# Optimization experiments

Measured on AMD Instinct MI355X. Metric: run time of the kernel, lower is better.

Reference implementation:

```python
import jax, jax.numpy as jnp
import numpy as np
import math

SQRT5 = math.sqrt(5.0)


def setup_inputs() -> dict:
    key = jax.random.key(0)
    k1, k2, k3, k4 = jax.random.split(key, 4)
    N1, N2, D = 8192, 8192, 64
    X1 = jax.random.normal(k1, (N1, D), dtype=jnp.float32)
    X2 = jax.random.normal(k2, (N2, D), dtype=jnp.float32)
    # positive scaling / lengthscale, kept away from 0 for numerical sanity
    c = jax.random.uniform(k3, (1,), dtype=jnp.float32) + 0.5
    l = jax.random.uniform(k4, (D,), dtype=jnp.float32) + 0.5
    return {"X1": X1, "X2": X2, "c": c, "l": l}


def _matern52(X1, X2, c, l):
    X1_l = X1 / l  # [N1, D]
    X2_l = X2 / l  # [N2, D]
    # pairwise Euclidean distance via the expansion ||a-b||^2 = ||a||^2 + ||b||^2 - 2 a.b
    # (avoids materializing the [N1, N2, D] broadcasted difference tensor)
    sq1 = jnp.sum(X1_l * X1_l, axis=-1)  # [N1]
    sq2 = jnp.sum(X2_l * X2_l, axis=-1)  # [N2]
    cross = jnp.einsum("nd,md->nm", X1_l, X2_l)  # [N1, N2]
    d2 = jnp.maximum(sq1[:, None] + sq2[None, :] - 2.0 * cross, 0.0)
    r = jnp.sqrt(d2)  # [N1, N2]
    c2 = jnp.squeeze(c * c)
    return c2 * (1.0 + SQRT5 * r + (5.0 / 3.0) * (r * r)) * jnp.exp(-SQRT5 * r)


def reference(X1, X2, c, l):
    return _matern52(X1, X2, c, l)
```

## Files before the change

### kernel.cpp

```cpp
#include <hip/hip_runtime.h>
#include <math.h>

#define N_DIM 64
#define TILE  128

typedef unsigned short ushort_t;
typedef unsigned int   uint_t;
typedef _Float16 f16x8 __attribute__((ext_vector_type(8)));
typedef _Float16 f16x4 __attribute__((ext_vector_type(4)));
typedef float    f32x4 __attribute__((ext_vector_type(4)));

__device__ __forceinline__ int swz16(int row, int kc) {
    return (row << 7) + ((kc ^ (row & 7)) << 4);
}

typedef __attribute__((address_space(1))) const void gas_void;
typedef __attribute__((address_space(3))) void       las_void;
__device__ __forceinline__ void gload16(const void* g, void* l) {
    __builtin_amdgcn_global_load_lds((gas_void*)g, (las_void*)l, 16, 0, 0);
}

__global__ __launch_bounds__(256)
void matern52_prep_kernel(const float* __restrict__ X,
                          const float* __restrict__ l,
                          unsigned char* __restrict__ dst,
                          float* __restrict__ sq, int N)
{
    const int t   = threadIdx.x;
    const int kq  = t & 15;
    const int row = blockIdx.x * 16 + (t >> 4);

    float4 lv = *reinterpret_cast<const float4*>(&l[kq * 4]);
    float4 x  = *reinterpret_cast<const float4*>(&X[(size_t)row * N_DIM + kq * 4]);
    const float a0 = x.x / lv.x, a1 = x.y / lv.y, a2 = x.z / lv.z, a3 = x.w / lv.w;

    float s = a0 * a0;
    s = fmaf(a1, a1, s); s = fmaf(a2, a2, s); s = fmaf(a3, a3, s);
    s += __shfl_xor(s, 1);
    s += __shfl_xor(s, 2);
    s += __shfl_xor(s, 4);
    s += __shfl_xor(s, 8);
    if (kq == 0) sq[row] = s;

    f16x4 h = { (_Float16)a0, (_Float16)a1, (_Float16)a2, (_Float16)a3 };
    const int off = (row << 7) + ((((kq >> 1) ^ (row & 7))) << 4) + ((kq & 1) << 3);
    *reinterpret_cast<f16x4*>(dst + off) = h;
}

__global__ __launch_bounds__(256, 4)
void matern52_main_kernel(const unsigned char* __restrict__ A16,
                          const unsigned char* __restrict__ B16,
                          const float* __restrict__ sq1,
                          const float* __restrict__ sq2,
                          const float* __restrict__ cc,
                          float* __restrict__ out,
                          int N1, int N2)
{
    __shared__ __align__(16) unsigned char lds[2 * TILE * N_DIM * 2];

    const int t  = threadIdx.x;
    const int bi = blockIdx.y, bj = blockIdx.x;

    unsigned char* ldsA = lds;
    unsigned char* ldsB = lds + TILE * N_DIM * 2;

    {
        const unsigned char* srcA = A16 + (size_t)bi * (TILE * N_DIM * 2);
        const unsigned char* srcB = B16 + (size_t)bj * (TILE * N_DIM * 2);
        const int wbase = (t >> 6) << 10;
        const int gb    = t * 16;
        #pragma unroll
        for (int i = 0; i < 4; ++i) {
            gload16(srcA + i * 4096 + gb, ldsA + i * 4096 + wbase);
            gload16(srcB + i * 4096 + gb, ldsB + i * 4096 + wbase);
        }
    }
    __syncthreads();

    const int wid  = t >> 6;
    const int lane = t & 63;
    const int wtr  = wid >> 1;
    const int wtc  = wid & 1;
    const int fr   = lane & 15;
    const int kg   = lane >> 4;

    f32x4 acc[4][4] = {};

    #pragma unroll
    for (int kk = 0; kk < 2; ++kk) {
        f16x8 af[4], bg[4];
        #pragma unroll
        for (int m = 0; m < 4; ++m)
            af[m] = *reinterpret_cast<const f16x8*>(
                ldsA + swz16(wtr * 64 + m * 16 + fr, kk * 4 + kg));
        #pragma unroll
        for (int n = 0; n < 4; ++n)
            bg[n] = *reinterpret_cast<const f16x8*>(
                ldsB + swz16(wtc * 64 + n * 16 + fr, kk * 4 + kg));
        #pragma unroll
        for (int m = 0; m < 4; ++m)
            #pragma unroll
            for (int n = 0; n < 4; ++n)
                acc[m][n] = __builtin_amdgcn_mfma_f32_16x16x32_f16(
                    bg[n], af[m], acc[m][n], 0, 0, 0);
    }

    const float c0 = cc[0];
    const float SQ5    = 2.23606797749979f;
    const float FIVE3  = 1.66666666666667f;
    const float NK     = -3.22617785847899f;
    const float l2c2   = 2.885390081777927f * __logf(c0);

    const float* sqA = sq1 + bi * TILE;
    const float* sqB = sq2 + bj * TILE + wtc * 64;

    #pragma unroll
    for (int m = 0; m < 4; ++m) {
        const int row_l = wtr * 64 + m * 16 + fr;
        const float sa = sqA[row_l];
        float* rowp = out + ((size_t)(bi * TILE) + row_l) * (size_t)N2
                          + (size_t)(bj * TILE) + wtc * 64;
        #pragma unroll
        for (int n = 0; n < 4; ++n) {
            const int cb = n * 16 + kg * 4;
            f32x4 sb4 = *reinterpret_cast<const f32x4*>(sqB + cb);
            f32x4 v = acc[m][n];
            f32x4 res;
            #pragma unroll
            for (int q = 0; q < 4; ++q) {
                float d2 = fmaxf(fmaf(-2.0f, v[q], sa + sb4[q]), 0.0f);
                float r  = __builtin_amdgcn_sqrtf(d2);
                float e  = __builtin_amdgcn_exp2f(fmaf(NK, r, l2c2));
                res[q] = fmaf(FIVE3, d2, fmaf(SQ5, r, 1.0f)) * e;
            }
            *reinterpret_cast<f32x4*>(rowp + cb) = res;
        }
    }
}

__device__ __forceinline__ ushort_t f2bf(float f) {
    uint_t u = __float_as_uint(f);
    u += 0x7FFFu + ((u >> 16) & 1u);
    return (ushort_t)(u >> 16);
}
__device__ __forceinline__ float bf2f(ushort_t h) {
    return __uint_as_float(((uint_t)h) << 16);
}
typedef short s16x8 __attribute__((ext_vector_type(8)));

__global__ __launch_bounds__(512, 4)
void matern52_fallback_kernel(const float* __restrict__ X1,
                              const float* __restrict__ X2,
                              const float* __restrict__ cc,
                              const float* __restrict__ l,
                              float* __restrict__ out,
                              int N1, int N2)
{
    __shared__ ushort_t Ah[TILE * N_DIM], Al[TILE * N_DIM];
    __shared__ ushort_t Bh[TILE * N_DIM], Bl[TILE * N_DIM];
    __shared__ float sqA[TILE], sqB[TILE];

    const int t  = threadIdx.x;
    const int bi = blockIdx.y, bj = blockIdx.x;
    const int kq   = t & 15;
    const int rsub = t >> 4;

    float4 lv = *reinterpret_cast<const float4*>(&l[kq * 4]);
    const float rlx = 1.f / lv.x, rly = 1.f / lv.y, rlz = 1.f / lv.z, rlw = 1.f / lv.w;
    const float* x1b = X1 + (size_t)(bi * TILE) * N_DIM;
    const float* x2b = X2 + (size_t)(bj * TILE) * N_DIM;

    #define STAGE(Xb, Th, Tl, SQ)                                              \
    {                                                                          \
        _Pragma("unroll")                                                      \
        for (int c = 0; c < 4; ++c) {                                          \
            const int row = c * 32 + rsub;                                     \
            float4 x = *reinterpret_cast<const float4*>(&(Xb)[row * N_DIM + kq * 4]); \
            float a0 = x.x * rlx, a1 = x.y * rly, a2 = x.z * rlz, a3 = x.w * rlw; \
            ushort_t h0 = f2bf(a0), h1 = f2bf(a1), h2 = f2bf(a2), h3 = f2bf(a3); \
            ushort_t e0 = f2bf(a0 - bf2f(h0)), e1 = f2bf(a1 - bf2f(h1));       \
            ushort_t e2 = f2bf(a2 - bf2f(h2)), e3 = f2bf(a3 - bf2f(h3));       \
            const int off = (row << 7) + (((kq >> 1) << 4) ^ ((row & 7) << 4)) + ((kq & 1) << 3); \
            uint2 hv, lvv;                                                     \
            hv.x  = (uint_t)h0 | ((uint_t)h1 << 16);                           \
            hv.y  = (uint_t)h2 | ((uint_t)h3 << 16);                           \
            lvv.x = (uint_t)e0 | ((uint_t)e1 << 16);                           \
            lvv.y = (uint_t)e2 | ((uint_t)e3 << 16);                           \
            *reinterpret_cast<uint2*>((char*)(Th) + off) = hv;                 \
            *reinterpret_cast<uint2*>((char*)(Tl) + off) = lvv;                \
            float s = a0 * a0;                                                 \
            s = fmaf(a1, a1, s); s = fmaf(a2, a2, s); s = fmaf(a3, a3, s);     \
            s += __shfl_xor(s, 1);                                             \
            s += __shfl_xor(s, 2);                                             \
            s += __shfl_xor(s, 4);                                             \
            s += __shfl_xor(s, 8);                                             \
            if (kq == 0) (SQ)[row] = s;                                        \
        }                                                                      \
    }
    STAGE(x1b, Ah, Al, sqA)
    STAGE(x2b, Bh, Bl, sqB)
    #undef STAGE
    __syncthreads();

    const int wid  = t >> 6;
    const int lane = t & 63;
    const int wtr = wid >> 1, wtc = wid & 1;
    const int fr  = lane & 15, kg = lane >> 4;

    f32x4 acc[2][4] = {};
    #pragma unroll
    for (int pass = 0; pass < 3; ++pass) {
        const ushort_t* TA = (pass == 2) ? Al : Ah;
        const ushort_t* TB = (pass == 1) ? Bl : Bh;
        #pragma unroll
        for (int kk = 0; kk < 2; ++kk) {
            s16x8 af[2], bg[4];
            #pragma unroll
            for (int m = 0; m < 2; ++m)
                af[m] = *reinterpret_cast<const s16x8*>(
                    (const char*)TA + swz16(wtr * 32 + m * 16 + fr, kk * 4 + kg));
            #pragma unroll
            for (int n = 0; n < 4; ++n)
                bg[n] = *reinterpret_cast<const s16x8*>(
                    (const char*)TB + swz16(wtc * 64 + n * 16 + fr, kk * 4 + kg));
            #pragma unroll
            for (int m = 0; m < 2; ++m)
                #pragma unroll
                for (int n = 0; n < 4; ++n)
                    acc[m][n] = __builtin_amdgcn_mfma_f32_16x16x32_bf16(
                        bg[n], af[m], acc[m][n], 0, 0, 0);
        }
    }

    const float c0 = cc[0];
    const float SQ5   = 2.23606797749979f;
    const float FIVE3 = 1.66666666666667f;
    const float lnc2  = 2.0f * __logf(c0);

    #pragma unroll
    for (int m = 0; m < 2; ++m) {
        const int row_l = wtr * 32 + m * 16 + fr;
        const float sa = sqA[row_l];
        float* rowp = out + ((size_t)(bi * TILE) + row_l) * (size_t)N2
                          + (size_t)(bj * TILE) + wtc * 64;
        #pragma unroll
        for (int n = 0; n < 4; ++n) {
            const int cb = n * 16 + kg * 4;
            f32x4 sb4 = *reinterpret_cast<const f32x4*>(&sqB[wtc * 64 + cb]);
            f32x4 v = acc[m][n];
            f32x4 res;
            #pragma unroll
            for (int q = 0; q < 4; ++q) {
                float d2 = fmaxf(fmaf(-2.0f, v[q], sa + sb4[q]), 0.0f);
                float r  = sqrtf(d2);
                float e  = __expf(fmaf(-SQ5, r, lnc2));
                res[q] = fmaf(FIVE3, d2, fmaf(SQ5, r, 1.0f)) * e;
            }
            *reinterpret_cast<f32x4*>(rowp + cb) = res;
        }
    }
}

extern "C" void kernel_launch(void* const* d_in, const int* in_sizes, int n_in,
                              void* d_out, int out_size, void* d_ws, size_t ws_size,
                              hipStream_t stream) {
    const float* X1 = (const float*)d_in[0];
    const float* X2 = (const float*)d_in[1];
    const float* c  = (const float*)d_in[2];
    const float* l  = (const float*)d_in[3];
    float* out = (float*)d_out;

    const int N1 = in_sizes[0] / N_DIM;
    const int N2 = in_sizes[1] / N_DIM;

    const size_t aBytes = (size_t)N1 * 128;
    const size_t bBytes = (size_t)N2 * 128;
    const size_t needWs = aBytes + bBytes + (size_t)(N1 + N2) * sizeof(float);

    dim3 grid(N2 / TILE, N1 / TILE);

    if (ws_size >= needWs) {
        unsigned char* A16 = (unsigned char*)d_ws;
        unsigned char* B16 = A16 + aBytes;
        float* sq1 = (float*)(B16 + bBytes);
        float* sq2 = sq1 + N1;

        matern52_prep_kernel<<<dim3(N1 / 16), 256, 0, stream>>>(X1, l, A16, sq1, N1);
        matern52_prep_kernel<<<dim3(N2 / 16), 256, 0, stream>>>(X2, l, B16, sq2, N2);
        matern52_main_kernel<<<grid, 256, 0, stream>>>(A16, B16, sq1, sq2, c, out, N1, N2);
    } else {
        matern52_fallback_kernel<<<grid, 512, 0, stream>>>(X1, X2, c, l, out, N1, N2);
    }
}
```

Baseline: 58.13 us.

## Read f16 operands directly from global memory and use nontemporal output stores

The main kernel no longer stages A/B tiles into LDS through global_load_lds with a swizzled layout and a barrier. Each lane now loads its MFMA fragments straight from global memory, which relies on L1/L2 caching of the small f16 operand arrays. The prep kernel writes a plain row-major layout to match. Output stores become nontemporal to avoid polluting cache with the 256MB result. The trade-off is redundant global/L2 traffic for operand fragments, since each tile is read by several waves, in exchange for dropping the LDS staging and the sync.

```diff
diff --git a/kernel.cpp b/kernel.cpp
--- a/kernel.cpp
+++ b/kernel.cpp
@@ -9,16 +9,6 @@
 typedef _Float16 f16x8 __attribute__((ext_vector_type(8)));
 typedef _Float16 f16x4 __attribute__((ext_vector_type(4)));
 typedef float    f32x4 __attribute__((ext_vector_type(4)));
-
-__device__ __forceinline__ int swz16(int row, int kc) {
-    return (row << 7) + ((kc ^ (row & 7)) << 4);
-}
-
-typedef __attribute__((address_space(1))) const void gas_void;
-typedef __attribute__((address_space(3))) void       las_void;
-__device__ __forceinline__ void gload16(const void* g, void* l) {
-    __builtin_amdgcn_global_load_lds((gas_void*)g, (las_void*)l, 16, 0, 0);
-}
 
 __global__ __launch_bounds__(256)
 void matern52_prep_kernel(const float* __restrict__ X,
@@ -43,8 +33,7 @@
     if (kq == 0) sq[row] = s;
 
     f16x4 h = { (_Float16)a0, (_Float16)a1, (_Float16)a2, (_Float16)a3 };
-    const int off = (row << 7) + ((((kq >> 1) ^ (row & 7))) << 4) + ((kq & 1) << 3);
-    *reinterpret_cast<f16x4*>(dst + off) = h;
+    *reinterpret_cast<f16x4*>(dst + (size_t)row * 128 + kq * 8) = h;
 }
 
 __global__ __launch_bounds__(256, 4)
@@ -56,27 +45,8 @@
                           float* __restrict__ out,
                           int N1, int N2)
 {
-    __shared__ __align__(16) unsigned char lds[2 * TILE * N_DIM * 2];
-
-    const int t  = threadIdx.x;
-    const int bi = blockIdx.y, bj = blockIdx.x;
-
-    unsigned char* ldsA = lds;
-    unsigned char* ldsB = lds + TILE * N_DIM * 2;
-
-    {
-        const unsigned char* srcA = A16 + (size_t)bi * (TILE * N_DIM * 2);
-        const unsigned char* srcB = B16 + (size_t)bj * (TILE * N_DIM * 2);
-        const int wbase = (t >> 6) << 10;
-        const int gb    = t * 16;
-        #pragma unroll
-        for (int i = 0; i < 4; ++i) {
-            gload16(srcA + i * 4096 + gb, ldsA + i * 4096 + wbase);
-            gload16(srcB + i * 4096 + gb, ldsB + i * 4096 + wbase);
-        }
-    }
-    __syncthreads();
-
+    const int t    = threadIdx.x;
+    const int bi   = blockIdx.y, bj = blockIdx.x;
     const int wid  = t >> 6;
     const int lane = t & 63;
     const int wtr  = wid >> 1;
@@ -84,6 +54,11 @@
     const int fr   = lane & 15;
     const int kg   = lane >> 4;
 
+    const unsigned char* pa =
+        A16 + (size_t)bi * (TILE * 128) + ((wtr * 64 + fr) << 7) + (kg << 4);
+    const unsigned char* pb =
+        B16 + (size_t)bj * (TILE * 128) + ((wtc * 64 + fr) << 7) + (kg << 4);
+
     f32x4 acc[4][4] = {};
 
     #pragma unroll
@@ -91,12 +66,10 @@
         f16x8 af[4], bg[4];
         #pragma unroll
         for (int m = 0; m < 4; ++m)
-            af[m] = *reinterpret_cast<const f16x8*>(
-                ldsA + swz16(wtr * 64 + m * 16 + fr, kk * 4 + kg));
+            af[m] = *reinterpret_cast<const f16x8*>(pa + m * 2048 + kk * 64);
         #pragma unroll
         for (int n = 0; n < 4; ++n)
-            bg[n] = *reinterpret_cast<const f16x8*>(
-                ldsB + swz16(wtc * 64 + n * 16 + fr, kk * 4 + kg));
+            bg[n] = *reinterpret_cast<const f16x8*>(pb + n * 2048 + kk * 64);
         #pragma unroll
         for (int m = 0; m < 4; ++m)
             #pragma unroll
@@ -106,10 +79,10 @@
     }
 
     const float c0 = cc[0];
-    const float SQ5    = 2.23606797749979f;
-    const float FIVE3  = 1.66666666666667f;
-    const float NK     = -3.22617785847899f;
-    const float l2c2   = 2.885390081777927f * __logf(c0);
+    const float SQ5   = 2.23606797749979f;
+    const float FIVE3 = 1.66666666666667f;
+    const float NK    = -3.22617785847899f;
+    const float l2c2  = 2.885390081777927f * __logf(c0);
 
     const float* sqA = sq1 + bi * TILE;
     const float* sqB = sq2 + bj * TILE + wtc * 64;
@@ -133,7 +106,7 @@
                 float e  = __builtin_amdgcn_exp2f(fmaf(NK, r, l2c2));
                 res[q] = fmaf(FIVE3, d2, fmaf(SQ5, r, 1.0f)) * e;
             }
-            *reinterpret_cast<f32x4*>(rowp + cb) = res;
+            __builtin_nontemporal_store(res, reinterpret_cast<f32x4*>(rowp + cb));
         }
     }
 }
@@ -147,6 +120,10 @@
     return __uint_as_float(((uint_t)h) << 16);
 }
 typedef short s16x8 __attribute__((ext_vector_type(8)));
+
+__device__ __forceinline__ int swz16(int row, int kc) {
+    return (row << 7) + ((kc ^ (row & 7)) << 4);
+}
 
 __global__ __launch_bounds__(512, 4)
 void matern52_fallback_kernel(const float* __restrict__ X1,
```

Result: slower. 91.62 us (+57.6%).

## Make main kernel persistent over four B tiles with double-buffered LDS prefetch

Applied to the files above, without the earlier changes.

Each 512-thread block now loads a 256-row A tile once and loops over four consecutive 128-column B tiles. Two B buffers let the next-next tile's global_load_lds overlap the epilogue of the current tile. This amortizes the A load and the launch/prologue cost across more output and hides B load latency behind the exp/sqrt epilogue and stores. In exchange the block uses 64 KB of LDS, which lowers occupancy, and there are fewer blocks (512 for the test shape). It also adds a shape guard that falls back to the old path for unsupported sizes.

```diff
diff --git a/kernel.cpp b/kernel.cpp
--- a/kernel.cpp
+++ b/kernel.cpp
@@ -3,6 +3,9 @@
 
 #define N_DIM 64
 #define TILE  128
+#define BM    256
+#define BN    128
+#define NTJ   4
 
 typedef unsigned short ushort_t;
 typedef unsigned int   uint_t;
@@ -47,32 +50,38 @@
     *reinterpret_cast<f16x4*>(dst + off) = h;
 }
 
-__global__ __launch_bounds__(256, 4)
+__global__ __launch_bounds__(512, 4)
 void matern52_main_kernel(const unsigned char* __restrict__ A16,
                           const unsigned char* __restrict__ B16,
                           const float* __restrict__ sq1,
                           const float* __restrict__ sq2,
                           const float* __restrict__ cc,
                           float* __restrict__ out,
-                          int N1, int N2)
+                          int N1, int N2, int njg)
 {
-    __shared__ __align__(16) unsigned char lds[2 * TILE * N_DIM * 2];
-
-    const int t  = threadIdx.x;
-    const int bi = blockIdx.y, bj = blockIdx.x;
-
+    __shared__ __align__(16) unsigned char lds[65536];
     unsigned char* ldsA = lds;
-    unsigned char* ldsB = lds + TILE * N_DIM * 2;
+
+    const int t    = threadIdx.x;
+    const int bi   = blockIdx.x / njg;
+    const int bjg  = blockIdx.x % njg;
+    const int bj0  = bjg * NTJ;
+
+    const int wbase = (t >> 6) << 10;
+    const int gb    = t * 16;
 
     {
-        const unsigned char* srcA = A16 + (size_t)bi * (TILE * N_DIM * 2);
-        const unsigned char* srcB = B16 + (size_t)bj * (TILE * N_DIM * 2);
-        const int wbase = (t >> 6) << 10;
-        const int gb    = t * 16;
-        #pragma unroll
-        for (int i = 0; i < 4; ++i) {
-            gload16(srcA + i * 4096 + gb, ldsA + i * 4096 + wbase);
-            gload16(srcB + i * 4096 + gb, ldsB + i * 4096 + wbase);
+        const unsigned char* srcA = A16 + (size_t)bi * (BM * 128);
+        #pragma unroll
+        for (int i = 0; i < 4; ++i)
+            gload16(srcA + i * 8192 + gb, ldsA + i * 8192 + wbase);
+        #pragma unroll
+        for (int j = 0; j < 2; ++j) {
+            const unsigned char* srcB = B16 + (size_t)(bj0 + j) * (BN * 128);
+            unsigned char* ldsB = lds + 32768 + j * 16384;
+            #pragma unroll
+            for (int i = 0; i < 2; ++i)
+                gload16(srcB + i * 8192 + gb, ldsB + i * 8192 + wbase);
         }
     }
     __syncthreads();
@@ -84,56 +93,71 @@
     const int fr   = lane & 15;
     const int kg   = lane >> 4;
 
-    f32x4 acc[4][4] = {};
+    const float c0 = cc[0];
+    const float SQ5   = 2.23606797749979f;
+    const float FIVE3 = 1.66666666666667f;
+    const float NK    = -3.22617785847899f;
+    const float l2c2  = 2.885390081777927f * __logf(c0);
+
+    const float* sqA = sq1 + bi * BM;
 
     #pragma unroll
-    for (int kk = 0; kk < 2; ++kk) {
-        f16x8 af[4], bg[4];
-        #pragma unroll
-        for (int m = 0; m < 4; ++m)
-            af[m] = *reinterpret_cast<const f16x8*>(
-                ldsA + swz16(wtr * 64 + m * 16 + fr, kk * 4 + kg));
-        #pragma unroll
-        for (int n = 0; n < 4; ++n)
-            bg[n] = *reinterpret_cast<const f16x8*>(
-                ldsB + swz16(wtc * 64 + n * 16 + fr, kk * 4 + kg));
-        #pragma unroll
-        for (int m = 0; m < 4; ++m)
+    for (int j = 0; j < NTJ; ++j) {
+        unsigned char* ldsB = lds + 32768 + (j & 1) * 16384;
+
+        f32x4 acc[4][4] = {};
+        #pragma unroll
+        for (int kk = 0; kk < 2; ++kk) {
+            f16x8 af[4], bg[4];
+            #pragma unroll
+            for (int m = 0; m < 4; ++m)
+                af[m] = *reinterpret_cast<const f16x8*>(
+                    ldsA + swz16(wtr * 64 + m * 16 + fr, kk * 4 + kg));
             #pragma unroll
             for (int n = 0; n < 4; ++n)
-                acc[m][n] = __builtin_amdgcn_mfma_f32_16x16x32_f16(
-                    bg[n], af[m], acc[m][n], 0, 0, 0);
-    }
-
-    const float c0 = cc[0];
-    const float SQ5    = 2.23606797749979f;
-    const float FIVE3  = 1.66666666666667f;
-    const float NK     = -3.22617785847899f;
-    const float l2c2   = 2.885390081777927f * __logf(c0);
-
-    const float* sqA = sq1 + bi * TILE;
-    const float* sqB = sq2 + bj * TILE + wtc * 64;
-
-    #pragma unroll
-    for (int m = 0; m < 4; ++m) {
-        const int row_l = wtr * 64 + m * 16 + fr;
-        const float sa = sqA[row_l];
-        float* rowp = out + ((size_t)(bi * TILE) + row_l) * (size_t)N2
-                          + (size_t)(bj * TILE) + wtc * 64;
-        #pragma unroll
-        for (int n = 0; n < 4; ++n) {
-            const int cb = n * 16 + kg * 4;
-            f32x4 sb4 = *reinterpret_cast<const f32x4*>(sqB + cb);
-            f32x4 v = acc[m][n];
-            f32x4 res;
-            #pragma unroll
-            for (int q = 0; q < 4; ++q) {
-                float d2 = fmaxf(fmaf(-2.0f, v[q], sa + sb4[q]), 0.0f);
-                float r  = __builtin_amdgcn_sqrtf(d2);
-                float e  = __builtin_amdgcn_exp2f(fmaf(NK, r, l2c2));
-                res[q] = fmaf(FIVE3, d2, fmaf(SQ5, r, 1.0f)) * e;
+                bg[n] = *reinterpret_cast<const f16x8*>(
+                    ldsB + swz16(wtc * 64 + n * 16 + fr, kk * 4 + kg));
+            #pragma unroll
+            for (int m = 0; m < 4; ++m)
+                #pragma unroll
+                for (int n = 0; n < 4; ++n)
+                    acc[m][n] = __builtin_amdgcn_mfma_f32_16x16x32_f16(
+                        bg[n], af[m], acc[m][n], 0, 0, 0);
+        }
+
+        __syncthreads();
+
+        if (j < NTJ - 2) {
+            const unsigned char* srcB = B16 + (size_t)(bj0 + j + 2) * (BN * 128);
+            #pragma unroll
+            for (int i = 0; i < 2; ++i)
+                gload16(srcB + i * 8192 + gb, ldsB + i * 8192 + wbase);
+        }
+
+        const int bj = bj0 + j;
+        const float* sqB = sq2 + bj * BN + wtc * 64;
+
+        #pragma unroll
+        for (int m = 0; m < 4; ++m) {
+            const int row_l = wtr * 64 + m * 16 + fr;
+            const float sa = sqA[row_l];
+            float* rowp = out + ((size_t)(bi * BM) + row_l) * (size_t)N2
+                              + (size_t)(bj * BN) + wtc * 64;
+            #pragma unroll
+            for (int n = 0; n < 4; ++n) {
+                const int cb = n * 16 + kg * 4;
+                f32x4 sb4 = *reinterpret_cast<const f32x4*>(sqB + cb);
+                f32x4 v = acc[m][n];
+                f32x4 res;
+                #pragma unroll
+                for (int q = 0; q < 4; ++q) {
+                    float d2 = fmaxf(fmaf(-2.0f, v[q], sa + sb4[q]), 0.0f);
+                    float r  = __builtin_amdgcn_sqrtf(d2);
+                    float e  = __builtin_amdgcn_exp2f(fmaf(NK, r, l2c2));
+                    res[q] = fmaf(FIVE3, d2, fmaf(SQ5, r, 1.0f)) * e;
+                }
+                *reinterpret_cast<f32x4*>(rowp + cb) = res;
             }
-            *reinterpret_cast<f32x4*>(rowp + cb) = res;
         }
     }
 }
@@ -277,9 +301,10 @@
     const size_t bBytes = (size_t)N2 * 128;
     const size_t needWs = aBytes + bBytes + (size_t)(N1 + N2) * sizeof(float);
 
-    dim3 grid(N2 / TILE, N1 / TILE);
-
-    if (ws_size >= needWs) {
+    const bool shapeOK = (N1 % BM == 0) && (N2 % (BN * NTJ) == 0) &&
+                         (N1 % 16 == 0) && (N2 % 16 == 0);
+
+    if (ws_size >= needWs && shapeOK) {
         unsigned char* A16 = (unsigned char*)d_ws;
         unsigned char* B16 = A16 + aBytes;
         float* sq1 = (float*)(B16 + bBytes);
@@ -287,8 +312,13 @@
 
         matern52_prep_kernel<<<dim3(N1 / 16), 256, 0, stream>>>(X1, l, A16, sq1, N1);
         matern52_prep_kernel<<<dim3(N2 / 16), 256, 0, stream>>>(X2, l, B16, sq2, N2);
-        matern52_main_kernel<<<grid, 256, 0, stream>>>(A16, B16, sq1, sq2, c, out, N1, N2);
+
+        const int njg  = N2 / (BN * NTJ);
+        const int nblk = (N1 / BM) * njg;
+        matern52_main_kernel<<<dim3(nblk), 512, 0, stream>>>(
+            A16, B16, sq1, sq2, c, out, N1, N2, njg);
     } else {
+        dim3 grid(N2 / TILE, N1 / TILE);
         matern52_fallback_kernel<<<grid, 512, 0, stream>>>(X1, X2, c, l, out, N1, N2);
     }
 }
```

After: 64.70 us. 11.3% more time.

## Merge prep launches and remap main-kernel blocks for XCD-local tile grouping

Applied to the files above, without the earlier changes.

Combines the two prep kernel launches into a single launch that covers both X1 and X2 rows, which removes one launch and its gap. The main kernel now runs on a 1D grid whose block IDs are remapped so that the blocks landing on each of the 8 XCDs (round-robin dispatch) cover a contiguous range of tiles, improving L2 reuse of the A/B fp16 operands. A shape check is added that routes non-conforming sizes to the fallback kernel.

```diff
diff --git a/kernel.cpp b/kernel.cpp
--- a/kernel.cpp
+++ b/kernel.cpp
@@ -21,14 +21,24 @@
 }
 
 __global__ __launch_bounds__(256)
-void matern52_prep_kernel(const float* __restrict__ X,
+void matern52_prep_kernel(const float* __restrict__ X1,
+                          const float* __restrict__ X2,
                           const float* __restrict__ l,
-                          unsigned char* __restrict__ dst,
-                          float* __restrict__ sq, int N)
+                          unsigned char* __restrict__ dstA,
+                          unsigned char* __restrict__ dstB,
+                          float* __restrict__ sq1,
+                          float* __restrict__ sq2,
+                          int N1)
 {
-    const int t   = threadIdx.x;
-    const int kq  = t & 15;
-    const int row = blockIdx.x * 16 + (t >> 4);
+    const int t  = threadIdx.x;
+    const int kq = t & 15;
+    int row = blockIdx.x * 16 + (t >> 4);
+
+    const float* __restrict__ X;
+    unsigned char* __restrict__ dst;
+    float* __restrict__ sq;
+    if (row < N1) { X = X1; dst = dstA; sq = sq1; }
+    else          { X = X2; dst = dstB; sq = sq2; row -= N1; }
 
     float4 lv = *reinterpret_cast<const float4*>(&l[kq * 4]);
     float4 x  = *reinterpret_cast<const float4*>(&X[(size_t)row * N_DIM + kq * 4]);
@@ -54,19 +64,23 @@
                           const float* __restrict__ sq2,
                           const float* __restrict__ cc,
                           float* __restrict__ out,
-                          int N1, int N2)
+                          int N1, int N2, int nbx, int chunk)
 {
     __shared__ __align__(16) unsigned char lds[2 * TILE * N_DIM * 2];
 
-    const int t  = threadIdx.x;
-    const int bi = blockIdx.y, bj = blockIdx.x;
+    const int t = threadIdx.x;
+
+    const int orig  = blockIdx.x;
+    const int newid = (orig & 7) * chunk + (orig >> 3);
+    const int bi    = newid / nbx;
+    const int bj    = newid % nbx;
 
     unsigned char* ldsA = lds;
     unsigned char* ldsB = lds + TILE * N_DIM * 2;
 
     {
-        const unsigned char* srcA = A16 + (size_t)bi * (TILE * N_DIM * 2);
-        const unsigned char* srcB = B16 + (size_t)bj * (TILE * N_DIM * 2);
+        const unsigned char* srcA = A16 + (size_t)bi * (TILE * 128);
+        const unsigned char* srcB = B16 + (size_t)bj * (TILE * 128);
         const int wbase = (t >> 6) << 10;
         const int gb    = t * 16;
         #pragma unroll
@@ -106,10 +120,10 @@
     }
 
     const float c0 = cc[0];
-    const float SQ5    = 2.23606797749979f;
-    const float FIVE3  = 1.66666666666667f;
-    const float NK     = -3.22617785847899f;
-    const float l2c2   = 2.885390081777927f * __logf(c0);
+    const float SQ5   = 2.23606797749979f;
+    const float FIVE3 = 1.66666666666667f;
+    const float NK    = -3.22617785847899f;
+    const float l2c2  = 2.885390081777927f * __logf(c0);
 
     const float* sqA = sq1 + bi * TILE;
     const float* sqB = sq2 + bj * TILE + wtc * 64;
@@ -277,18 +291,26 @@
     const size_t bBytes = (size_t)N2 * 128;
     const size_t needWs = aBytes + bBytes + (size_t)(N1 + N2) * sizeof(float);
 
-    dim3 grid(N2 / TILE, N1 / TILE);
-
-    if (ws_size >= needWs) {
+    const int nby  = N1 / TILE;
+    const int nbx  = N2 / TILE;
+    const int nblk = nby * nbx;
+
+    const bool shapeOK = (N1 % TILE == 0) && (N2 % TILE == 0) &&
+                         (N1 % 16 == 0) && (nblk % 8 == 0);
+
+    if (ws_size >= needWs && shapeOK) {
         unsigned char* A16 = (unsigned char*)d_ws;
         unsigned char* B16 = A16 + aBytes;
         float* sq1 = (float*)(B16 + bBytes);
         float* sq2 = sq1 + N1;
 
-        matern52_prep_kernel<<<dim3(N1 / 16), 256, 0, stream>>>(X1, l, A16, sq1, N1);
-        matern52_prep_kernel<<<dim3(N2 / 16), 256, 0, stream>>>(X2, l, B16, sq2, N2);
-        matern52_main_kernel<<<grid, 256, 0, stream>>>(A16, B16, sq1, sq2, c, out, N1, N2);
+        matern52_prep_kernel<<<dim3((N1 + N2) / 16), 256, 0, stream>>>(
+            X1, X2, l, A16, B16, sq1, sq2, N1);
+
+        matern52_main_kernel<<<dim3(nblk), 256, 0, stream>>>(
+            A16, B16, sq1, sq2, c, out, N1, N2, nbx, nblk / 8);
     } else {
+        dim3 grid(N2 / TILE, N1 / TILE);
         matern52_fallback_kernel<<<grid, 512, 0, stream>>>(X1, X2, c, l, out, N1, N2);
     }
 }
```

Result: no change. 58.94 us (+1.4%).
